# Kernel tuning notes

Hardware: AMD Instinct MI355X
Metric: run time of the kernel (lower is better)

Reference implementation:

```python
import jax, jax.numpy as jnp
import numpy as np

NODE = 100000
REL = 2000
E = 600000  # n_edges == triple_size
D = 128
DEPTH = 2
HEADS = 1


def setup_inputs() -> dict:
    key = jax.random.key(0)
    ks = jax.random.split(key, 8)
    features = jax.random.normal(ks[0], (NODE, D), jnp.float32)
    rel_emb = jax.random.normal(ks[1], (REL, D), jnp.float32)
    sp_val = jax.random.uniform(ks[2], (E,), jnp.float32)
    attn_kernels = jax.random.normal(ks[3], (DEPTH, HEADS, 3 * D), jnp.float32) * 0.1
    adj_src = jnp.sort(jax.random.randint(ks[4], (E,), 0, NODE))  # tf.segment_sum needs sorted ids
    adj_dst = jax.random.randint(ks[5], (E,), 0, NODE)
    sp_rel = jax.random.randint(ks[6], (E,), 0, REL)
    sp_row = jnp.arange(E)  # sparse (triple, rel) matrix row indices
    return dict(features=features, rel_emb=rel_emb, sp_val=sp_val,
                attn_kernels=attn_kernels, adj_src=adj_src, adj_dst=adj_dst,
                sp_rel=sp_rel, sp_row=sp_row)


def _segment_softmax(logits, seg, num):
    m = jax.ops.segment_max(logits, seg, num_segments=num)
    e = jnp.exp(logits - m[seg])
    s = jax.ops.segment_sum(e, seg, num_segments=num)
    return e / s[seg]


def reference(features, rel_emb, sp_val, attn_kernels, adj_src, adj_dst, sp_rel, sp_row):
    act = jax.nn.relu
    feats = act(features)
    outputs = [feats]
    for l in range(DEPTH):
        heads = []
        for h in range(HEADS):
            ak = attn_kernels[l, h]  # [3D]
            # sparse (triple x rel) @ rel_emb -> per-edge relation embedding [E, D]
            rels = jax.ops.segment_sum(sp_val[:, None] * rel_emb[sp_rel], sp_row,
                                       num_segments=E)
            # tf.nn.l2_normalize with eps 1e-12
            rels = rels * jax.lax.rsqrt(jnp.maximum(jnp.sum(rels * rels, axis=1,
                                                            keepdims=True), 1e-12))
            neighs = feats[adj_dst]  # [E, D]
            selfs = feats[adj_src]   # [E, D]
            # Householder-style reflection of neighbor features across rels
            proj = jnp.sum(neighs * rels, axis=1, keepdims=True) * rels
            neighs = neighs - 2.0 * proj
            # attention logits: concat([selfs, neighs, rels]) @ ak
            att = selfs @ ak[:D] + neighs @ ak[D:2 * D] + rels @ ak[2 * D:]
            a = _segment_softmax(att, adj_src, NODE)  # tf.sparse_softmax per row
            heads.append(jax.ops.segment_sum(neighs * a[:, None], adj_src,
                                             num_segments=NODE))
        feats = heads[0] if HEADS == 1 else jnp.concatenate(heads, axis=1)
        feats = act(feats)
        outputs.append(feats)
    return jnp.concatenate(outputs, axis=1)  # [NODE, D*(DEPTH+1)]
```

## Files before the change

kernel.cpp:

```cpp
#include <hip/hip_runtime.h>
#include <math.h>

#define NNODE 100000
#define NREL 2000
#define NEDGE 600000
#define DIM 128
#define NDEPTH 2
#define OUTC 384

#define RELU_BLOCKS 12500
#define PRE_BLOCKS 500
#define ROW_BLOCKS ((NNODE + 1 + 255) / 256)

__device__ __forceinline__ float wave_sum(float v) {
#pragma unroll
    for (int off = 32; off > 0; off >>= 1)
        v += __shfl_xor(v, off, 64);
    return v;
}

__device__ __forceinline__ unsigned short f2bf(float f) {
    unsigned b = __float_as_uint(f);
    return (unsigned short)((b + 0x7fffu + ((b >> 16) & 1u)) >> 16);
}
__device__ __forceinline__ unsigned pack2(float f0, float f1) {
    return (unsigned)f2bf(f0) | ((unsigned)f2bf(f1) << 16);
}
__device__ __forceinline__ void unpack2(unsigned u, float& lo, float& hi) {
    lo = __uint_as_float(u << 16);
    hi = __uint_as_float(u & 0xffff0000u);
}

__global__ void k_setup(const float* __restrict__ f, const float* __restrict__ rel,
                        const float* __restrict__ attn, const int* __restrict__ adj_src,
                        float* __restrict__ out, unsigned short* __restrict__ fm,
                        unsigned short* __restrict__ relm,
                        float* __restrict__ relnorm2, float* __restrict__ rdB,
                        float* __restrict__ rdC,
                        float* __restrict__ selfdot0, float* __restrict__ neighdot0,
                        int* __restrict__ row_ptr) {
    int b = blockIdx.x;
    if (b < RELU_BLOCKS) {
        int idx = b * 256 + threadIdx.x;
        int n = idx >> 5;
        int q = idx & 31;
        float4 v = reinterpret_cast<const float4*>(f + (size_t)n * DIM)[q];
        v.x = fmaxf(v.x, 0.f); v.y = fmaxf(v.y, 0.f);
        v.z = fmaxf(v.z, 0.f); v.w = fmaxf(v.w, 0.f);
        reinterpret_cast<float4*>(out + (size_t)n * OUTC)[q] = v;
        uint2 p;
        p.x = pack2(v.x, v.y);
        p.y = pack2(v.z, v.w);
        reinterpret_cast<uint2*>(fm + (size_t)n * DIM)[q] = p;
        float4 a = reinterpret_cast<const float4*>(attn)[q];
        float4 bb = reinterpret_cast<const float4*>(attn + DIM)[q];
        float pa = v.x * a.x + v.y * a.y + v.z * a.z + v.w * a.w;
        float pb = v.x * bb.x + v.y * bb.y + v.z * bb.z + v.w * bb.w;
#pragma unroll
        for (int off = 1; off <= 16; off <<= 1) {
            pa += __shfl_xor(pa, off, 64);
            pb += __shfl_xor(pb, off, 64);
        }
        if (q == 0) { selfdot0[n] = pa; neighdot0[n] = pb; }
    } else if (b < RELU_BLOCKS + PRE_BLOCKS) {
        int wid = (b - RELU_BLOCKS) * 4 + (threadIdx.x >> 6);
        int lane = threadIdx.x & 63;
        float2 v = reinterpret_cast<const float2*>(rel + (size_t)wid * DIM)[lane];
        reinterpret_cast<unsigned*>(relm + (size_t)wid * DIM)[lane] = pack2(v.x, v.y);
        float2 b0 = reinterpret_cast<const float2*>(attn + DIM)[lane];
        float2 c0 = reinterpret_cast<const float2*>(attn + 2 * DIM)[lane];
        float2 b1 = reinterpret_cast<const float2*>(attn + 3 * DIM + DIM)[lane];
        float2 c1 = reinterpret_cast<const float2*>(attn + 3 * DIM + 2 * DIM)[lane];
        float n2  = wave_sum(v.x * v.x + v.y * v.y);
        float pb0 = wave_sum(v.x * b0.x + v.y * b0.y);
        float pc0 = wave_sum(v.x * c0.x + v.y * c0.y);
        float pb1 = wave_sum(v.x * b1.x + v.y * b1.y);
        float pc1 = wave_sum(v.x * c1.x + v.y * c1.y);
        if (lane == 0) {
            relnorm2[wid] = n2;
            rdB[wid] = pb0;        rdC[wid] = pc0;
            rdB[NREL + wid] = pb1; rdC[NREL + wid] = pc1;
        }
    } else {
        int n = (b - RELU_BLOCKS - PRE_BLOCKS) * 256 + threadIdx.x;
        if (n <= NNODE) {
            int lo = 0, hi = NEDGE;
            while (lo < hi) {
                int mid = (lo + hi) >> 1;
                if (adj_src[mid] < n) lo = mid + 1; else hi = mid;
            }
            row_ptr[n] = lo;
        }
    }
}

__global__ void k_gat(const unsigned short* __restrict__ fin_m,
                      float* __restrict__ fout,
                      unsigned short* __restrict__ fout_m,
                      const unsigned short* __restrict__ relm,
                      const int* __restrict__ adj_dst, const int* __restrict__ sp_rel,
                      const float* __restrict__ sp_val, const float* __restrict__ relnorm2,
                      const float* __restrict__ selfdot, const float* __restrict__ neighdot,
                      const float* __restrict__ rdB, const float* __restrict__ rdC,
                      const int* __restrict__ row_ptr,
                      float* __restrict__ selfdot_n, float* __restrict__ neighdot_n,
                      const float* __restrict__ ak_next, const int write_next) {
    int wid = (blockIdx.x * blockDim.x + threadIdx.x) >> 6;
    int lane = threadIdx.x & 63;
    if (wid >= NNODE) return;
    int g  = lane >> 4;
    int gl = lane & 15;
    int e0 = row_ptr[wid], e1 = row_ptr[wid + 1];

    float acc[8];
#pragma unroll
    for (int i = 0; i < 8; ++i) acc[i] = 0.f;
    float m = -3.0e38f, s = 0.f;
    float sd = selfdot[wid];

    int e = e0 + g;
    uint4 fb = make_uint4(0, 0, 0, 0), rb = make_uint4(0, 0, 0, 0);
    float ab = 0.f, qb = 0.f, q2 = 0.f;
    if (e < e1) {
        int dst = adj_dst[e], r = sp_rel[e];
        float v = sp_val[e];
        float sc = v * rsqrtf(fmaxf(v * v * relnorm2[r], 1e-12f));
        fb = reinterpret_cast<const uint4*>(fin_m + (size_t)dst * DIM)[gl];
        rb = reinterpret_cast<const uint4*>(relm + (size_t)r * DIM)[gl];
        float s2 = 2.f * sc * sc;
        ab = neighdot[dst] + sc * rdC[r];
        qb = s2 * rdB[r];
        q2 = s2;
    }
    while (e < e1) {
        int en = e + 4;
        uint4 fb2 = make_uint4(0, 0, 0, 0), rb2 = make_uint4(0, 0, 0, 0);
        float ab2 = 0.f, qb2 = 0.f, q22 = 0.f;
        if (en < e1) {
            int dst = adj_dst[en], r = sp_rel[en];
            float v = sp_val[en];
            float sc = v * rsqrtf(fmaxf(v * v * relnorm2[r], 1e-12f));
            fb2 = reinterpret_cast<const uint4*>(fin_m + (size_t)dst * DIM)[gl];
            rb2 = reinterpret_cast<const uint4*>(relm + (size_t)r * DIM)[gl];
            float s2 = 2.f * sc * sc;
            ab2 = neighdot[dst] + sc * rdC[r];
            qb2 = s2 * rdB[r];
            q22 = s2;
        }
        float f[8], rv[8];
        unpack2(fb.x, f[0], f[1]); unpack2(fb.y, f[2], f[3]);
        unpack2(fb.z, f[4], f[5]); unpack2(fb.w, f[6], f[7]);
        unpack2(rb.x, rv[0], rv[1]); unpack2(rb.y, rv[2], rv[3]);
        unpack2(rb.z, rv[4], rv[5]); unpack2(rb.w, rv[6], rv[7]);
        float dot = 0.f;
#pragma unroll
        for (int i = 0; i < 8; ++i) dot += f[i] * rv[i];
        dot += __shfl_xor(dot, 1, 64);
        dot += __shfl_xor(dot, 2, 64);
        dot += __shfl_xor(dot, 4, 64);
        dot += __shfl_xor(dot, 8, 64);
        float att = sd + ab - dot * qb;
        float k2 = dot * q2;
        float nm = fmaxf(m, att);
        float corr = __expf(m - nm);
        float w = __expf(att - nm);
        s = s * corr + w;
#pragma unroll
        for (int i = 0; i < 8; ++i)
            acc[i] = acc[i] * corr + w * (f[i] - k2 * rv[i]);
        m = nm;
        e = en; fb = fb2; rb = rb2; ab = ab2; qb = qb2; q2 = q22;
    }

#pragma unroll
    for (int off = 16; off <= 32; off <<= 1) {
        float mo = __shfl_xor(m, off, 64);
        float so = __shfl_xor(s, off, 64);
        float ao[8];
#pragma unroll
        for (int i = 0; i < 8; ++i) ao[i] = __shfl_xor(acc[i], off, 64);
        float nm = fmaxf(m, mo);
        float wa = __expf(m - nm), wb = __expf(mo - nm);
        s = s * wa + so * wb;
#pragma unroll
        for (int i = 0; i < 8; ++i) acc[i] = acc[i] * wa + ao[i] * wb;
        m = nm;
    }

    if (g == 0) {
        float inv = (s > 0.f) ? 1.f / s : 0.f;
        float o[8];
#pragma unroll
        for (int i = 0; i < 8; ++i) o[i] = fmaxf(acc[i] * inv, 0.f);
        float4* op = reinterpret_cast<float4*>(fout + (size_t)wid * OUTC) + gl * 2;
        op[0] = make_float4(o[0], o[1], o[2], o[3]);
        op[1] = make_float4(o[4], o[5], o[6], o[7]);
        if (write_next) {
            uint4 mw;
            mw.x = pack2(o[0], o[1]); mw.y = pack2(o[2], o[3]);
            mw.z = pack2(o[4], o[5]); mw.w = pack2(o[6], o[7]);
            reinterpret_cast<uint4*>(fout_m + (size_t)wid * DIM)[gl] = mw;
            const float4* aA = reinterpret_cast<const float4*>(ak_next) + gl * 2;
            const float4* aB = reinterpret_cast<const float4*>(ak_next + DIM) + gl * 2;
            float4 a0 = aA[0], a1 = aA[1], b0 = aB[0], b1 = aB[1];
            float pa = o[0] * a0.x + o[1] * a0.y + o[2] * a0.z + o[3] * a0.w
                     + o[4] * a1.x + o[5] * a1.y + o[6] * a1.z + o[7] * a1.w;
            float pb = o[0] * b0.x + o[1] * b0.y + o[2] * b0.z + o[3] * b0.w
                     + o[4] * b1.x + o[5] * b1.y + o[6] * b1.z + o[7] * b1.w;
#pragma unroll
            for (int off = 1; off <= 8; off <<= 1) {
                pa += __shfl_xor(pa, off, 64);
                pb += __shfl_xor(pb, off, 64);
            }
            if (gl == 0) { selfdot_n[wid] = pa; neighdot_n[wid] = pb; }
        }
    }
}

extern "C" void kernel_launch(void* const* d_in, const int* in_sizes, int n_in,
                              void* d_out, int out_size, void* d_ws, size_t ws_size,
                              hipStream_t stream) {
    const float* features = (const float*)d_in[0];
    const float* rel_emb  = (const float*)d_in[1];
    const float* sp_val   = (const float*)d_in[2];
    const float* attn     = (const float*)d_in[3];
    const int*   adj_src  = (const int*)d_in[4];
    const int*   adj_dst  = (const int*)d_in[5];
    const int*   sp_rel   = (const int*)d_in[6];
    float* out = (float*)d_out;

    char* p = (char*)d_ws;
    unsigned short* mir0 = (unsigned short*)p; p += (size_t)NNODE * DIM * 2;
    unsigned short* mir1 = (unsigned short*)p; p += (size_t)NNODE * DIM * 2;
    unsigned short* relm = (unsigned short*)p; p += (size_t)NREL * DIM * 2;
    float* sd0      = (float*)p; p += (size_t)NNODE * 4;
    float* nd0      = (float*)p; p += (size_t)NNODE * 4;
    float* sd1      = (float*)p; p += (size_t)NNODE * 4;
    float* nd1      = (float*)p; p += (size_t)NNODE * 4;
    float* relnorm2 = (float*)p; p += (size_t)NREL * 4;
    float* rdB      = (float*)p; p += (size_t)2 * NREL * 4;
    float* rdC      = (float*)p; p += (size_t)2 * NREL * 4;
    int*   row_ptr  = (int*)p;   p += (size_t)(NNODE + 1) * 4;

    k_setup<<<RELU_BLOCKS + PRE_BLOCKS + ROW_BLOCKS, 256, 0, stream>>>(
        features, rel_emb, attn, adj_src, out, mir0, relm,
        relnorm2, rdB, rdC, sd0, nd0, row_ptr);

    k_gat<<<(NNODE * 64 + 255) / 256, 256, 0, stream>>>(
        mir0, out + DIM, mir1, relm, adj_dst, sp_rel, sp_val, relnorm2,
        sd0, nd0, rdB, rdC, row_ptr, sd1, nd1, attn + 3 * DIM, 1);

    k_gat<<<(NNODE * 64 + 255) / 256, 256, 0, stream>>>(
        mir1, out + 2 * DIM, (unsigned short*)nullptr, relm, adj_dst, sp_rel, sp_val, relnorm2,
        sd1, nd1, rdB + NREL, rdC + NREL, row_ptr,
        (float*)nullptr, (float*)nullptr, (const float*)nullptr, 0);
}
```

Baseline: 163.2 us.

## Map one node per 16-lane group and precompute packed per-edge scalars

Each k_gat wave now handles four nodes, one per 16-lane group, instead of splitting one node's edges across four groups. This removes the cross-group online-softmax merge shuffles and lets all lanes write output. A new k_edges kernel precomputes per-edge scale terms for both layers and packs dst and rel ids into one float4, so the inner loop does a single 16-byte load per edge. Packed float2 math is used for the dot and accumulate. The cost is an extra kernel and 19 MB of edge-data traffic. There is also more load imbalance, since each group walks its own node's edge list serially.

```diff
diff --git a/kernel.cpp b/kernel.cpp
--- a/kernel.cpp
+++ b/kernel.cpp
@@ -1,16 +1,18 @@
 #include <hip/hip_runtime.h>
 #include <math.h>
+#include <stdint.h>
 
 #define NNODE 100000
 #define NREL 2000
 #define NEDGE 600000
 #define DIM 128
-#define NDEPTH 2
 #define OUTC 384
 
 #define RELU_BLOCKS 12500
 #define PRE_BLOCKS 500
 #define ROW_BLOCKS ((NNODE + 1 + 255) / 256)
+
+typedef float f32x2 __attribute__((ext_vector_type(2)));
 
 __device__ __forceinline__ float wave_sum(float v) {
 #pragma unroll
@@ -26,9 +28,11 @@
 __device__ __forceinline__ unsigned pack2(float f0, float f1) {
     return (unsigned)f2bf(f0) | ((unsigned)f2bf(f1) << 16);
 }
-__device__ __forceinline__ void unpack2(unsigned u, float& lo, float& hi) {
-    lo = __uint_as_float(u << 16);
-    hi = __uint_as_float(u & 0xffff0000u);
+__device__ __forceinline__ f32x2 bf2(unsigned u) {
+    f32x2 r;
+    r.x = __uint_as_float(u << 16);
+    r.y = __uint_as_float(u & 0xffff0000u);
+    return r;
 }
 
 __global__ void k_setup(const float* __restrict__ f, const float* __restrict__ rel,
@@ -94,126 +98,147 @@
     }
 }
 
+__global__ void k_edges(const float* __restrict__ sp_val, const int* __restrict__ sp_rel,
+                        const int* __restrict__ adj_dst,
+                        const float* __restrict__ relnorm2,
+                        const float* __restrict__ rdB, const float* __restrict__ rdC,
+                        float4* __restrict__ ed0, float4* __restrict__ ed1) {
+    int e = blockIdx.x * blockDim.x + threadIdx.x;
+    if (e >= NEDGE) return;
+    float v = sp_val[e];
+    int r = sp_rel[e];
+    float n2 = relnorm2[r];
+    float sc = v * rsqrtf(fmaxf(v * v * n2, 1e-12f));
+    float q2 = 2.f * sc * sc;
+    unsigned pk = ((unsigned)adj_dst[e] << 11) | (unsigned)r;
+    float pkf = __uint_as_float(pk);
+    ed0[e] = make_float4(sc * rdC[r],        q2 * rdB[r],        q2, pkf);
+    ed1[e] = make_float4(sc * rdC[NREL + r], q2 * rdB[NREL + r], q2, pkf);
+}
+
+template<int USE_ED, int WRITE_NEXT>
 __global__ void k_gat(const unsigned short* __restrict__ fin_m,
                       float* __restrict__ fout,
                       unsigned short* __restrict__ fout_m,
                       const unsigned short* __restrict__ relm,
+                      const float4* __restrict__ edata,
                       const int* __restrict__ adj_dst, const int* __restrict__ sp_rel,
                       const float* __restrict__ sp_val, const float* __restrict__ relnorm2,
+                      const float* __restrict__ rdB, const float* __restrict__ rdC,
                       const float* __restrict__ selfdot, const float* __restrict__ neighdot,
-                      const float* __restrict__ rdB, const float* __restrict__ rdC,
                       const int* __restrict__ row_ptr,
-                      float* __restrict__ selfdot_n, float* __restrict__ neighdot_n,
-                      const float* __restrict__ ak_next, const int write_next) {
-    int wid = (blockIdx.x * blockDim.x + threadIdx.x) >> 6;
+                      float* __restrict__ sd_n, float* __restrict__ nd_n,
+                      const float* __restrict__ ak_next) {
+    int wv = (blockIdx.x * blockDim.x + threadIdx.x) >> 6;
     int lane = threadIdx.x & 63;
-    if (wid >= NNODE) return;
-    int g  = lane >> 4;
-    int gl = lane & 15;
-    int e0 = row_ptr[wid], e1 = row_ptr[wid + 1];
-
-    float acc[8];
-#pragma unroll
-    for (int i = 0; i < 8; ++i) acc[i] = 0.f;
+    int g = lane >> 4, gl = lane & 15;
+    int node = wv * 4 + g;
+    if (node >= NNODE) return;
+    int e0 = row_ptr[node], e1 = row_ptr[node + 1];
+    float sd = selfdot[node];
+
+    f32x2 acc0 = 0.f, acc1 = 0.f, acc2 = 0.f, acc3 = 0.f;
     float m = -3.0e38f, s = 0.f;
-    float sd = selfdot[wid];
-
-    int e = e0 + g;
+
     uint4 fb = make_uint4(0, 0, 0, 0), rb = make_uint4(0, 0, 0, 0);
     float ab = 0.f, qb = 0.f, q2 = 0.f;
+    int e = e0;
     if (e < e1) {
-        int dst = adj_dst[e], r = sp_rel[e];
-        float v = sp_val[e];
-        float sc = v * rsqrtf(fmaxf(v * v * relnorm2[r], 1e-12f));
-        fb = reinterpret_cast<const uint4*>(fin_m + (size_t)dst * DIM)[gl];
-        rb = reinterpret_cast<const uint4*>(relm + (size_t)r * DIM)[gl];
-        float s2 = 2.f * sc * sc;
-        ab = neighdot[dst] + sc * rdC[r];
-        qb = s2 * rdB[r];
-        q2 = s2;
+        int dst, r;
+        if (USE_ED) {
+            float4 ed = edata[e];
+            unsigned pk = __float_as_uint(ed.w);
+            dst = (int)(pk >> 11); r = (int)(pk & 2047u);
+            ab = sd + ed.x + neighdot[dst];
+            qb = ed.y; q2 = ed.z;
+        } else {
+            dst = adj_dst[e]; r = sp_rel[e];
+            float v = sp_val[e];
+            float sc = v * rsqrtf(fmaxf(v * v * relnorm2[r], 1e-12f));
+            q2 = 2.f * sc * sc;
+            qb = q2 * rdB[r];
+            ab = sd + sc * rdC[r] + neighdot[dst];
+        }
+        fb = *reinterpret_cast<const uint4*>(fin_m + (size_t)dst * DIM + gl * 8);
+        rb = *reinterpret_cast<const uint4*>(relm + (size_t)r * DIM + gl * 8);
     }
     while (e < e1) {
-        int en = e + 4;
+        int en = e + 1;
+        bool more = en < e1;
         uint4 fb2 = make_uint4(0, 0, 0, 0), rb2 = make_uint4(0, 0, 0, 0);
         float ab2 = 0.f, qb2 = 0.f, q22 = 0.f;
-        if (en < e1) {
-            int dst = adj_dst[en], r = sp_rel[en];
-            float v = sp_val[en];
-            float sc = v * rsqrtf(fmaxf(v * v * relnorm2[r], 1e-12f));
-            fb2 = reinterpret_cast<const uint4*>(fin_m + (size_t)dst * DIM)[gl];
-            rb2 = reinterpret_cast<const uint4*>(relm + (size_t)r * DIM)[gl];
-            float s2 = 2.f * sc * sc;
-            ab2 = neighdot[dst] + sc * rdC[r];
-            qb2 = s2 * rdB[r];
-            q22 = s2;
-        }
-        float f[8], rv[8];
-        unpack2(fb.x, f[0], f[1]); unpack2(fb.y, f[2], f[3]);
-        unpack2(fb.z, f[4], f[5]); unpack2(fb.w, f[6], f[7]);
-        unpack2(rb.x, rv[0], rv[1]); unpack2(rb.y, rv[2], rv[3]);
-        unpack2(rb.z, rv[4], rv[5]); unpack2(rb.w, rv[6], rv[7]);
-        float dot = 0.f;
-#pragma unroll
-        for (int i = 0; i < 8; ++i) dot += f[i] * rv[i];
+        if (more) {
+            int dst, r;
+            if (USE_ED) {
+                float4 ed = edata[en];
+                unsigned pk = __float_as_uint(ed.w);
+                dst = (int)(pk >> 11); r = (int)(pk & 2047u);
+                ab2 = sd + ed.x + neighdot[dst];
+                qb2 = ed.y; q22 = ed.z;
+            } else {
+                dst = adj_dst[en]; r = sp_rel[en];
+                float v = sp_val[en];
+                float sc = v * rsqrtf(fmaxf(v * v * relnorm2[r], 1e-12f));
+                q22 = 2.f * sc * sc;
+                qb2 = q22 * rdB[r];
+                ab2 = sd + sc * rdC[r] + neighdot[dst];
+            }
+            fb2 = *reinterpret_cast<const uint4*>(fin_m + (size_t)dst * DIM + gl * 8);
+            rb2 = *reinterpret_cast<const uint4*>(relm + (size_t)r * DIM + gl * 8);
+        }
+        f32x2 f0 = bf2(fb.x), f1 = bf2(fb.y), f2 = bf2(fb.z), f3 = bf2(fb.w);
+        f32x2 r0 = bf2(rb.x), r1 = bf2(rb.y), r2 = bf2(rb.z), r3 = bf2(rb.w);
+        f32x2 d2 = f0 * r0;
+        d2 += f1 * r1;
+        d2 += f2 * r2;
+        d2 += f3 * r3;
+        float dot = d2.x + d2.y;
         dot += __shfl_xor(dot, 1, 64);
         dot += __shfl_xor(dot, 2, 64);
         dot += __shfl_xor(dot, 4, 64);
         dot += __shfl_xor(dot, 8, 64);
-        float att = sd + ab - dot * qb;
+        float att = ab - dot * qb;
         float k2 = dot * q2;
         float nm = fmaxf(m, att);
         float corr = __expf(m - nm);
         float w = __expf(att - nm);
         s = s * corr + w;
+        acc0 = acc0 * corr + w * (f0 - k2 * r0);
+        acc1 = acc1 * corr + w * (f1 - k2 * r1);
+        acc2 = acc2 * corr + w * (f2 - k2 * r2);
+        acc3 = acc3 * corr + w * (f3 - k2 * r3);
+        m = nm;
+        e = en;
+        fb = fb2; rb = rb2; ab = ab2; qb = qb2; q2 = q22;
+    }
+
+    float inv = (s > 0.f) ? 1.f / s : 0.f;
+    float o[8];
+    o[0] = fmaxf(acc0.x * inv, 0.f); o[1] = fmaxf(acc0.y * inv, 0.f);
+    o[2] = fmaxf(acc1.x * inv, 0.f); o[3] = fmaxf(acc1.y * inv, 0.f);
+    o[4] = fmaxf(acc2.x * inv, 0.f); o[5] = fmaxf(acc2.y * inv, 0.f);
+    o[6] = fmaxf(acc3.x * inv, 0.f); o[7] = fmaxf(acc3.y * inv, 0.f);
+    float4* op = reinterpret_cast<float4*>(fout + (size_t)node * OUTC + gl * 8);
+    op[0] = make_float4(o[0], o[1], o[2], o[3]);
+    op[1] = make_float4(o[4], o[5], o[6], o[7]);
+    if (WRITE_NEXT) {
+        uint4 mw;
+        mw.x = pack2(o[0], o[1]); mw.y = pack2(o[2], o[3]);
+        mw.z = pack2(o[4], o[5]); mw.w = pack2(o[6], o[7]);
+        *reinterpret_cast<uint4*>(fout_m + (size_t)node * DIM + gl * 8) = mw;
+        const float4* aA = reinterpret_cast<const float4*>(ak_next) + gl * 2;
+        const float4* aB = reinterpret_cast<const float4*>(ak_next + DIM) + gl * 2;
+        float4 a0 = aA[0], a1 = aA[1], b0 = aB[0], b1 = aB[1];
+        float pa = o[0] * a0.x + o[1] * a0.y + o[2] * a0.z + o[3] * a0.w
+                 + o[4] * a1.x + o[5] * a1.y + o[6] * a1.z + o[7] * a1.w;
+        float pb = o[0] * b0.x + o[1] * b0.y + o[2] * b0.z + o[3] * b0.w
+                 + o[4] * b1.x + o[5] * b1.y + o[6] * b1.z + o[7] * b1.w;
 #pragma unroll
-        for (int i = 0; i < 8; ++i)
-            acc[i] = acc[i] * corr + w * (f[i] - k2 * rv[i]);
-        m = nm;
-        e = en; fb = fb2; rb = rb2; ab = ab2; qb = qb2; q2 = q22;
-    }
-
-#pragma unroll
-    for (int off = 16; off <= 32; off <<= 1) {
-        float mo = __shfl_xor(m, off, 64);
-        float so = __shfl_xor(s, off, 64);
-        float ao[8];
-#pragma unroll
-        for (int i = 0; i < 8; ++i) ao[i] = __shfl_xor(acc[i], off, 64);
-        float nm = fmaxf(m, mo);
-        float wa = __expf(m - nm), wb = __expf(mo - nm);
-        s = s * wa + so * wb;
-#pragma unroll
-        for (int i = 0; i < 8; ++i) acc[i] = acc[i] * wa + ao[i] * wb;
-        m = nm;
-    }
-
-    if (g == 0) {
-        float inv = (s > 0.f) ? 1.f / s : 0.f;
-        float o[8];
-#pragma unroll
-        for (int i = 0; i < 8; ++i) o[i] = fmaxf(acc[i] * inv, 0.f);
-        float4* op = reinterpret_cast<float4*>(fout + (size_t)wid * OUTC) + gl * 2;
-        op[0] = make_float4(o[0], o[1], o[2], o[3]);
-        op[1] = make_float4(o[4], o[5], o[6], o[7]);
-        if (write_next) {
-            uint4 mw;
-            mw.x = pack2(o[0], o[1]); mw.y = pack2(o[2], o[3]);
-            mw.z = pack2(o[4], o[5]); mw.w = pack2(o[6], o[7]);
-            reinterpret_cast<uint4*>(fout_m + (size_t)wid * DIM)[gl] = mw;
-            const float4* aA = reinterpret_cast<const float4*>(ak_next) + gl * 2;
-            const float4* aB = reinterpret_cast<const float4*>(ak_next + DIM) + gl * 2;
-            float4 a0 = aA[0], a1 = aA[1], b0 = aB[0], b1 = aB[1];
-            float pa = o[0] * a0.x + o[1] * a0.y + o[2] * a0.z + o[3] * a0.w
-                     + o[4] * a1.x + o[5] * a1.y + o[6] * a1.z + o[7] * a1.w;
-            float pb = o[0] * b0.x + o[1] * b0.y + o[2] * b0.z + o[3] * b0.w
-                     + o[4] * b1.x + o[5] * b1.y + o[6] * b1.z + o[7] * b1.w;
-#pragma unroll
-            for (int off = 1; off <= 8; off <<= 1) {
-                pa += __shfl_xor(pa, off, 64);
-                pb += __shfl_xor(pb, off, 64);
-            }
-            if (gl == 0) { selfdot_n[wid] = pa; neighdot_n[wid] = pb; }
-        }
+        for (int off = 1; off <= 8; off <<= 1) {
+            pa += __shfl_xor(pa, off, 64);
+            pb += __shfl_xor(pb, off, 64);
+        }
+        if (gl == 0) { sd_n[node] = pa; nd_n[node] = pb; }
     }
 }
 
@@ -241,17 +266,35 @@
     float* rdB      = (float*)p; p += (size_t)2 * NREL * 4;
     float* rdC      = (float*)p; p += (size_t)2 * NREL * 4;
     int*   row_ptr  = (int*)p;   p += (size_t)(NNODE + 1) * 4;
+    p = (char*)(((uintptr_t)p + 15) & ~(uintptr_t)15);
+    float4* ed0 = (float4*)p; p += (size_t)NEDGE * 16;
+    float4* ed1 = (float4*)p; p += (size_t)NEDGE * 16;
+    size_t needed = (size_t)(p - (char*)d_ws);
+    bool use_ed = (ws_size >= needed);
 
     k_setup<<<RELU_BLOCKS + PRE_BLOCKS + ROW_BLOCKS, 256, 0, stream>>>(
         features, rel_emb, attn, adj_src, out, mir0, relm,
         relnorm2, rdB, rdC, sd0, nd0, row_ptr);
 
-    k_gat<<<(NNODE * 64 + 255) / 256, 256, 0, stream>>>(
-        mir0, out + DIM, mir1, relm, adj_dst, sp_rel, sp_val, relnorm2,
-        sd0, nd0, rdB, rdC, row_ptr, sd1, nd1, attn + 3 * DIM, 1);
-
-    k_gat<<<(NNODE * 64 + 255) / 256, 256, 0, stream>>>(
-        mir1, out + 2 * DIM, (unsigned short*)nullptr, relm, adj_dst, sp_rel, sp_val, relnorm2,
-        sd1, nd1, rdB + NREL, rdC + NREL, row_ptr,
-        (float*)nullptr, (float*)nullptr, (const float*)nullptr, 0);
-}
+    int gat_blocks = (NNODE / 4 * 64) / 256;
+
+    if (use_ed) {
+        k_edges<<<(NEDGE + 255) / 256, 256, 0, stream>>>(
+            sp_val, sp_rel, adj_dst, relnorm2, rdB, rdC, ed0, ed1);
+        k_gat<1, 1><<<gat_blocks, 256, 0, stream>>>(
+            mir0, out + DIM, mir1, relm, ed0, adj_dst, sp_rel, sp_val, relnorm2,
+            rdB, rdC, sd0, nd0, row_ptr, sd1, nd1, attn + 3 * DIM);
+        k_gat<1, 0><<<gat_blocks, 256, 0, stream>>>(
+            mir1, out + 2 * DIM, (unsigned short*)nullptr, relm, ed1, adj_dst, sp_rel,
+            sp_val, relnorm2, rdB + NREL, rdC + NREL, sd1, nd1, row_ptr,
+            (float*)nullptr, (float*)nullptr, (const float*)nullptr);
+    } else {
+        k_gat<0, 1><<<gat_blocks, 256, 0, stream>>>(
+            mir0, out + DIM, mir1, relm, (const float4*)nullptr, adj_dst, sp_rel,
+            sp_val, relnorm2, rdB, rdC, sd0, nd0, row_ptr, sd1, nd1, attn + 3 * DIM);
+        k_gat<0, 0><<<gat_blocks, 256, 0, stream>>>(
+            mir1, out + 2 * DIM, (unsigned short*)nullptr, relm, (const float4*)nullptr,
+            adj_dst, sp_rel, sp_val, relnorm2, rdB + NREL, rdC + NREL, sd1, nd1, row_ptr,
+            (float*)nullptr, (float*)nullptr, (const float*)nullptr);
+    }
+}
```

Result: faster. 144.3 us (-11.6%).
